# Kernel optimization log

Measured on AMD Instinct MI355X. Metric: run time of the kernel, lower is better.

The kernel has to match this reference:

```python
import jax, jax.numpy as jnp
import numpy as np

N = 20000       # nodes
E = 320000      # edges (without self-loops)
D_IN = 256
HID = 64        # per-head channels, layer 1
HEADS = 4
D_OUT = 256
EPS = 1e-5      # LayerNorm eps
SLOPE = 0.2     # LeakyReLU negative slope (PyG GATConv default)


def setup_inputs() -> dict:
    key = jax.random.key(0)
    ks = jax.random.split(key, 10)
    def glorot(k, shape):
        fan_in, fan_out = shape[0], int(np.prod(shape[1:]))
        s = np.sqrt(2.0 / (fan_in + fan_out)).astype(np.float32)
        return jax.random.normal(k, shape, dtype=jnp.float32) * s
    x = jax.random.normal(ks[0], (N, D_IN), dtype=jnp.float32)
    edge_index = jax.random.randint(ks[1], (2, E), 0, N, dtype=jnp.int64)
    return {
        "x": x,
        "edge_index": edge_index,
        # layer 1: GATConv(D_IN, HID, heads=4, concat=True)
        "W1": glorot(ks[2], (D_IN, HEADS * HID)),
        "a1_src": glorot(ks[3], (HEADS, HID)),
        "a1_dst": glorot(ks[4], (HEADS, HID)),
        "b1": jnp.zeros((HEADS * HID,), jnp.float32),
        # LayerNorm(HEADS*HID)
        "ln_g": jnp.ones((HEADS * HID,), jnp.float32),
        "ln_b": jnp.zeros((HEADS * HID,), jnp.float32),
        # layer 2: GATConv(HEADS*HID, D_OUT, heads=1, concat=False)
        "W2": glorot(ks[5], (HEADS * HID, D_OUT)),
        "a2_src": glorot(ks[6], (1, D_OUT)),
        "a2_dst": glorot(ks[7], (1, D_OUT)),
        "b2": jnp.zeros((D_OUT,), jnp.float32),
    }


def _gat(x, src, dst, W, a_src, a_dst, b, heads, ch, concat):
    """PyG-style GATConv (self-loops already appended to src/dst)."""
    n = x.shape[0]
    h = (x @ W).reshape(n, heads, ch)                      # [n,H,C]
    es = (h * a_src).sum(-1)                               # [n,H] src logits
    ed = (h * a_dst).sum(-1)                               # [n,H] dst logits
    e = jax.nn.leaky_relu(es[src] + ed[dst], SLOPE)        # [Etot,H]
    # softmax over incoming edges of each dst node (stable)
    m = jax.ops.segment_max(e, dst, num_segments=n)
    w = jnp.exp(e - m[dst])
    den = jax.ops.segment_sum(w, dst, num_segments=n)
    alpha = w / den[dst]                                   # [Etot,H]
    msg = h[src] * alpha[:, :, None]                       # [Etot,H,C]
    out = jax.ops.segment_sum(msg, dst, num_segments=n)    # [n,H,C]
    out = out.reshape(n, heads * ch) if concat else out.mean(axis=1)
    return out + b


def _layernorm(x, g, b):
    mu = x.mean(-1, keepdims=True)
    v = ((x - mu) ** 2).mean(-1, keepdims=True)
    return (x - mu) * jax.lax.rsqrt(v + EPS) * g + b


def reference(x, edge_index, W1, a1_src, a1_dst, b1, ln_g, ln_b, W2, a2_src, a2_dst, b2):
    loops = jnp.arange(N, dtype=edge_index.dtype)
    src = jnp.concatenate([edge_index[0], loops])
    dst = jnp.concatenate([edge_index[1], loops])
    h = _gat(x, src, dst, W1, a1_src, a1_dst, b1, HEADS, HID, True)
    h = jax.nn.relu(_layernorm(h, ln_g, ln_b))             # dropout is identity in eval
    out = _gat(h, src, dst, W2, a2_src, a2_dst, b2, 1, D_OUT, False)
    return out
```

## Files before the change

### kernel.cpp

```cpp
#include <hip/hip_runtime.h>
#include <hip/hip_bf16.h>
#include <math.h>

#define N_NODES 20000
#define N_EDGES 320000
#define N_ETOT  (N_EDGES + N_NODES)
#define SLOPE 0.2f
#define LN_EPS 1e-5f
#define APPEND_BLOCKS 1329
#define SLOTS 128

typedef __attribute__((ext_vector_type(8))) short short8v;
typedef __attribute__((ext_vector_type(4))) float f32x4;

__device__ __forceinline__ float lrelu(float x) { return x > 0.f ? x : SLOPE * x; }

__device__ __forceinline__ float rlf(float v, int l) {
  return __uint_as_float(__builtin_amdgcn_readlane(__float_as_uint(v), l));
}
__device__ __forceinline__ int rli(int v, int l) { return __builtin_amdgcn_readlane(v, l); }

__device__ __forceinline__ unsigned short f2bf(float f) {
  __hip_bfloat16 h = __float2bfloat16(f);
  return *reinterpret_cast<unsigned short*>(&h);
}
__device__ __forceinline__ float bf2f(unsigned short u) {
  return __uint_as_float(((unsigned int)u) << 16);
}

__global__ __launch_bounds__(256) void k_init(const float* __restrict__ W1, const float* __restrict__ W2,
                                              unsigned short* __restrict__ P1, unsigned short* __restrict__ P2,
                                              int* __restrict__ deg) {
  int b = blockIdx.x, t = threadIdx.x;
  if (b < 256) {
    int e = b * 256 + t;
    int j = e & 7, lane = (e >> 3) & 63, nf = (e >> 9) & 15, ks = (e >> 13) & 7;
    int col = nf * 16 + (lane & 15);
    int k = ks * 32 + (lane >> 4) * 8 + j;
    P1[e] = f2bf(W1[k * 256 + col]);
    P2[e] = f2bf(W2[k * 256 + col]);
  } else {
    int i = (b - 256) * 256 + t;
    if (i < N_NODES) deg[i] = 0;
  }
}

__global__ __launch_bounds__(256) void k_append_gemm1(const int* __restrict__ ei, int* __restrict__ deg,
                                                      int* __restrict__ srcs,
                                                      const float* __restrict__ x,
                                                      const unsigned short* __restrict__ Wp,
                                                      const float* __restrict__ asrc,
                                                      const float* __restrict__ adst,
                                                      unsigned short* __restrict__ C,
                                                      float* __restrict__ es, float* __restrict__ ed) {
  int b = blockIdx.x, tid = threadIdx.x;
  if (b < APPEND_BLOCKS) {
    int i = b * 256 + tid;
    if (i < N_ETOT) {
      int s, d;
      if (i < N_EDGES) { s = ei[i]; d = ei[N_EDGES + i]; } else { s = i - N_EDGES; d = s; }
      int slot = atomicAdd(&deg[d], 1);
      if (slot < SLOTS) srcs[d * SLOTS + slot] = s;
    }
    return;
  }
  int gwave = (b - APPEND_BLOCKS) * 4 + (tid >> 6);
  if (gwave >= 1250) return;
  int lane = tid & 63;
  int r = lane & 15, kg = lane >> 4;
  int rbase = gwave * 16;

  f32x4 acc[16];
#pragma unroll
  for (int i = 0; i < 16; ++i) acc[i] = (f32x4){0.f, 0.f, 0.f, 0.f};

#pragma unroll
  for (int ks = 0; ks < 8; ++ks) {
    int koff = ks * 32 + kg * 8;
    float4 lo = *reinterpret_cast<const float4*>(&x[(size_t)(rbase + r) * 256 + koff]);
    float4 hi = *reinterpret_cast<const float4*>(&x[(size_t)(rbase + r) * 256 + koff + 4]);
    short8v a;
    a[0] = (short)f2bf(lo.x); a[1] = (short)f2bf(lo.y); a[2] = (short)f2bf(lo.z); a[3] = (short)f2bf(lo.w);
    a[4] = (short)f2bf(hi.x); a[5] = (short)f2bf(hi.y); a[6] = (short)f2bf(hi.z); a[7] = (short)f2bf(hi.w);
#pragma unroll
    for (int nf = 0; nf < 16; ++nf) {
      int4 braw = *reinterpret_cast<const int4*>(&Wp[(size_t)(ks * 16 + nf) * 512 + lane * 8]);
      short8v bfr = __builtin_bit_cast(short8v, braw);
      acc[nf] = __builtin_amdgcn_mfma_f32_16x16x32_bf16(a, bfr, acc[nf], 0, 0, 0);
    }
  }

#pragma unroll
  for (int nf = 0; nf < 16; ++nf) {
#pragma unroll
    for (int q = 0; q < 4; ++q)
      C[(size_t)(rbase + kg * 4 + q) * 256 + nf * 16 + r] = f2bf(acc[nf][q]);
  }

  float as_v[16], ad_v[16];
#pragma unroll
  for (int nf = 0; nf < 16; ++nf) {
    as_v[nf] = asrc[nf * 16 + r];
    ad_v[nf] = adst[nf * 16 + r];
  }
#pragma unroll
  for (int q = 0; q < 4; ++q) {
    float hs[4], hd[4];
#pragma unroll
    for (int h = 0; h < 4; ++h) {
      hs[h] = 0.f; hd[h] = 0.f;
#pragma unroll
      for (int t = 0; t < 4; ++t) {
        int nf = h * 4 + t;
        hs[h] = fmaf(acc[nf][q], as_v[nf], hs[h]);
        hd[h] = fmaf(acc[nf][q], ad_v[nf], hd[h]);
      }
#pragma unroll
      for (int s = 1; s < 16; s <<= 1) {
        hs[h] += __shfl_xor(hs[h], s);
        hd[h] += __shfl_xor(hd[h], s);
      }
    }
    if (r == 0) {
      int row = rbase + kg * 4 + q;
#pragma unroll
      for (int h = 0; h < 4; ++h) {
        es[row * 4 + h] = hs[h];
        ed[row * 4 + h] = hd[h];
      }
    }
  }
}

__global__ __launch_bounds__(256) void k_gat1_gemm2(const unsigned short* __restrict__ h1,
                                                    const float* __restrict__ es, const float* __restrict__ ed,
                                                    const int* __restrict__ degv, const int* __restrict__ srcs,
                                                    const float* __restrict__ b1, const float* __restrict__ lng,
                                                    const float* __restrict__ lnb,
                                                    const unsigned short* __restrict__ Wp,
                                                    const float* __restrict__ a2s, const float* __restrict__ a2d,
                                                    unsigned short* __restrict__ h2b,
                                                    float* __restrict__ es2, float* __restrict__ ed2) {
  __shared__ char hm[16 * 512];
  __shared__ float esp[4][16], edp[4][16];
  int tid = threadIdx.x;
  int w = tid >> 6, lane = tid & 63;
  int myh = lane >> 4;
  int nbase = blockIdx.x * 16;

  for (int i = 0; i < 4; ++i) {
    int lrow = w * 4 + i;
    int n = nbase + lrow;
    int beg = n * SLOTS;
    int deg = degv[n]; deg = deg > SLOTS ? SLOTS : deg;
    float4 edv = *reinterpret_cast<const float4*>(&ed[n * 4]);
    float ax = 0.f, ay = 0.f, az = 0.f, aw = 0.f;
    float invden;

    if (deg <= 64) {
      int sv = 0;
      float e0 = -1e30f, e1 = -1e30f, e2 = -1e30f, e3 = -1e30f;
      bool valid = lane < deg;
      if (valid) {
        sv = srcs[beg + lane];
        float4 esv = *reinterpret_cast<const float4*>(&es[sv * 4]);
        e0 = lrelu(esv.x + edv.x); e1 = lrelu(esv.y + edv.y);
        e2 = lrelu(esv.z + edv.z); e3 = lrelu(esv.w + edv.w);
      }
      float m0 = e0, m1 = e1, m2 = e2, m3 = e3;
#pragma unroll
      for (int s = 1; s < 64; s <<= 1) {
        m0 = fmaxf(m0, __shfl_xor(m0, s)); m1 = fmaxf(m1, __shfl_xor(m1, s));
        m2 = fmaxf(m2, __shfl_xor(m2, s)); m3 = fmaxf(m3, __shfl_xor(m3, s));
      }
      float w0 = valid ? __expf(e0 - m0) : 0.f;
      float w1 = valid ? __expf(e1 - m1) : 0.f;
      float w2 = valid ? __expf(e2 - m2) : 0.f;
      float w3 = valid ? __expf(e3 - m3) : 0.f;
      float d0 = w0, d1 = w1, d2 = w2, d3 = w3;
#pragma unroll
      for (int s = 1; s < 64; s <<= 1) {
        d0 += __shfl_xor(d0, s); d1 += __shfl_xor(d1, s);
        d2 += __shfl_xor(d2, s); d3 += __shfl_xor(d3, s);
      }
      float den = (myh == 0) ? d0 : (myh == 1) ? d1 : (myh == 2) ? d2 : d3;
      invden = 1.f / den;

      int j = 0;
      for (; j + 8 <= deg; j += 8) {
        int ss[8]; ushort4 vv[8];
#pragma unroll
        for (int u = 0; u < 8; ++u) ss[u] = rli(sv, j + u);
#pragma unroll
        for (int u = 0; u < 8; ++u)
          vv[u] = *reinterpret_cast<const ushort4*>(&h1[(size_t)ss[u] * 256 + lane * 4]);
#pragma unroll
        for (int u = 0; u < 8; ++u) {
          int jj = j + u;
          float w0j = rlf(w0, jj), w1j = rlf(w1, jj), w2j = rlf(w2, jj), w3j = rlf(w3, jj);
          float wj = (myh == 0) ? w0j : (myh == 1) ? w1j : (myh == 2) ? w2j : w3j;
          ax = fmaf(wj, bf2f(vv[u].x), ax); ay = fmaf(wj, bf2f(vv[u].y), ay);
          az = fmaf(wj, bf2f(vv[u].z), az); aw = fmaf(wj, bf2f(vv[u].w), aw);
        }
      }
      for (; j + 4 <= deg; j += 4) {
        int ss[4]; ushort4 vv[4];
#pragma unroll
        for (int u = 0; u < 4; ++u) ss[u] = rli(sv, j + u);
#pragma unroll
        for (int u = 0; u < 4; ++u)
          vv[u] = *reinterpret_cast<const ushort4*>(&h1[(size_t)ss[u] * 256 + lane * 4]);
#pragma unroll
        for (int u = 0; u < 4; ++u) {
          int jj = j + u;
          float w0j = rlf(w0, jj), w1j = rlf(w1, jj), w2j = rlf(w2, jj), w3j = rlf(w3, jj);
          float wj = (myh == 0) ? w0j : (myh == 1) ? w1j : (myh == 2) ? w2j : w3j;
          ax = fmaf(wj, bf2f(vv[u].x), ax); ay = fmaf(wj, bf2f(vv[u].y), ay);
          az = fmaf(wj, bf2f(vv[u].z), az); aw = fmaf(wj, bf2f(vv[u].w), aw);
        }
      }
      for (; j < deg; ++j) {
        int sj = rli(sv, j);
        float w0j = rlf(w0, j), w1j = rlf(w1, j), w2j = rlf(w2, j), w3j = rlf(w3, j);
        float wj = (myh == 0) ? w0j : (myh == 1) ? w1j : (myh == 2) ? w2j : w3j;
        ushort4 v = *reinterpret_cast<const ushort4*>(&h1[(size_t)sj * 256 + lane * 4]);
        ax = fmaf(wj, bf2f(v.x), ax); ay = fmaf(wj, bf2f(v.y), ay);
        az = fmaf(wj, bf2f(v.z), az); aw = fmaf(wj, bf2f(v.w), aw);
      }
    } else {
      float m0 = -1e30f, m1 = -1e30f, m2 = -1e30f, m3 = -1e30f;
      for (int j = lane; j < deg; j += 64) {
        int s = srcs[beg + j];
        float4 esv = *reinterpret_cast<const float4*>(&es[s * 4]);
        m0 = fmaxf(m0, lrelu(esv.x + edv.x)); m1 = fmaxf(m1, lrelu(esv.y + edv.y));
        m2 = fmaxf(m2, lrelu(esv.z + edv.z)); m3 = fmaxf(m3, lrelu(esv.w + edv.w));
      }
#pragma unroll
      for (int s = 1; s < 64; s <<= 1) {
        m0 = fmaxf(m0, __shfl_xor(m0, s)); m1 = fmaxf(m1, __shfl_xor(m1, s));
        m2 = fmaxf(m2, __shfl_xor(m2, s)); m3 = fmaxf(m3, __shfl_xor(m3, s));
      }
      float edh = (myh == 0) ? edv.x : (myh == 1) ? edv.y : (myh == 2) ? edv.z : edv.w;
      float mh = (myh == 0) ? m0 : (myh == 1) ? m1 : (myh == 2) ? m2 : m3;
      float den = 0.f;
      for (int j = 0; j < deg; ++j) {
        int s = srcs[beg + j];
        float e = lrelu(es[s * 4 + myh] + edh);
        float wj = __expf(e - mh);
        den += wj;
        ushort4 v = *reinterpret_cast<const ushort4*>(&h1[(size_t)s * 256 + lane * 4]);
        ax = fmaf(wj, bf2f(v.x), ax); ay = fmaf(wj, bf2f(v.y), ay);
        az = fmaf(wj, bf2f(v.z), az); aw = fmaf(wj, bf2f(v.w), aw);
      }
      invden = 1.f / den;
    }

    float4 bb = *reinterpret_cast<const float4*>(&b1[lane * 4]);
    float vx = ax * invden + bb.x, vy = ay * invden + bb.y;
    float vz = az * invden + bb.z, vw = aw * invden + bb.w;
    float sum = vx + vy + vz + vw;
    float sq = vx * vx + vy * vy + vz * vz + vw * vw;
#pragma unroll
    for (int s = 1; s < 64; s <<= 1) { sum += __shfl_xor(sum, s); sq += __shfl_xor(sq, s); }
    float mu = sum * (1.f / 256.f);
    float var = sq * (1.f / 256.f) - mu * mu;
    float rstd = rsqrtf(var + LN_EPS);
    float4 g = *reinterpret_cast<const float4*>(&lng[lane * 4]);
    float4 lb = *reinterpret_cast<const float4*>(&lnb[lane * 4]);
    ushort4 o;
    o.x = f2bf(fmaxf(0.f, (vx - mu) * rstd * g.x + lb.x));
    o.y = f2bf(fmaxf(0.f, (vy - mu) * rstd * g.y + lb.y));
    o.z = f2bf(fmaxf(0.f, (vz - mu) * rstd * g.z + lb.z));
    o.w = f2bf(fmaxf(0.f, (vw - mu) * rstd * g.w + lb.w));
    *reinterpret_cast<ushort4*>(&hm[lrow * 512 + ((lane * 8 + lrow * 64) & 511)]) = o;
  }
  __syncthreads();

  int r = lane & 15, kg = lane >> 4;
  f32x4 acc[4];
#pragma unroll
  for (int i = 0; i < 4; ++i) acc[i] = (f32x4){0.f, 0.f, 0.f, 0.f};

#pragma unroll
  for (int ks = 0; ks < 8; ++ks) {
    int4 araw = *reinterpret_cast<const int4*>(
        &hm[r * 512 + (((ks * 64 + kg * 16) + r * 64) & 511)]);
    short8v a = __builtin_bit_cast(short8v, araw);
#pragma unroll
    for (int nf2 = 0; nf2 < 4; ++nf2) {
      int nf = w * 4 + nf2;
      int4 braw = *reinterpret_cast<const int4*>(&Wp[(size_t)(ks * 16 + nf) * 512 + lane * 8]);
      short8v bfr = __builtin_bit_cast(short8v, braw);
      acc[nf2] = __builtin_amdgcn_mfma_f32_16x16x32_bf16(a, bfr, acc[nf2], 0, 0, 0);
    }
  }

  int rbase = nbase;
#pragma unroll
  for (int nf2 = 0; nf2 < 4; ++nf2) {
#pragma unroll
    for (int q = 0; q < 4; ++q)
      h2b[(size_t)(rbase + kg * 4 + q) * 256 + w * 64 + nf2 * 16 + r] = f2bf(acc[nf2][q]);
  }

  float as_v[4], ad_v[4];
#pragma unroll
  for (int nf2 = 0; nf2 < 4; ++nf2) {
    as_v[nf2] = a2s[w * 64 + nf2 * 16 + r];
    ad_v[nf2] = a2d[w * 64 + nf2 * 16 + r];
  }
#pragma unroll
  for (int q = 0; q < 4; ++q) {
    float s0 = 0.f, d0 = 0.f;
#pragma unroll
    for (int nf2 = 0; nf2 < 4; ++nf2) {
      s0 = fmaf(acc[nf2][q], as_v[nf2], s0);
      d0 = fmaf(acc[nf2][q], ad_v[nf2], d0);
    }
#pragma unroll
    for (int s = 1; s < 16; s <<= 1) {
      s0 += __shfl_xor(s0, s);
      d0 += __shfl_xor(d0, s);
    }
    if (r == 0) {
      esp[w][kg * 4 + q] = s0;
      edp[w][kg * 4 + q] = d0;
    }
  }
  __syncthreads();
  if (tid < 16) {
    es2[rbase + tid] = esp[0][tid] + esp[1][tid] + esp[2][tid] + esp[3][tid];
    ed2[rbase + tid] = edp[0][tid] + edp[1][tid] + edp[2][tid] + edp[3][tid];
  }
}

__global__ __launch_bounds__(256) void k_gat2(const unsigned short* __restrict__ h2,
                                              const float* __restrict__ es, const float* __restrict__ ed,
                                              const int* __restrict__ degv, const int* __restrict__ srcs,
                                              const float* __restrict__ b2, float* __restrict__ out) {
  int n = (blockIdx.x * 256 + threadIdx.x) >> 6;
  if (n >= N_NODES) return;
  int lane = threadIdx.x & 63;
  int beg = n * SLOTS;
  int deg = degv[n]; deg = deg > SLOTS ? SLOTS : deg;
  float edn = ed[n];
  float ax = 0.f, ay = 0.f, az = 0.f, aw = 0.f;
  float invden;

  if (deg <= 64) {
    int sv = 0;
    float e = -1e30f;
    bool valid = lane < deg;
    if (valid) {
      sv = srcs[beg + lane];
      e = lrelu(es[sv] + edn);
    }
    float m = e;
#pragma unroll
    for (int s = 1; s < 64; s <<= 1) m = fmaxf(m, __shfl_xor(m, s));
    float wv = valid ? __expf(e - m) : 0.f;
    float den = wv;
#pragma unroll
    for (int s = 1; s < 64; s <<= 1) den += __shfl_xor(den, s);
    invden = 1.f / den;

    int j = 0;
    for (; j + 8 <= deg; j += 8) {
      int ss[8]; ushort4 vv[8]; float wj[8];
#pragma unroll
      for (int u = 0; u < 8; ++u) ss[u] = rli(sv, j + u);
#pragma unroll
      for (int u = 0; u < 8; ++u)
        vv[u] = *reinterpret_cast<const ushort4*>(&h2[(size_t)ss[u] * 256 + lane * 4]);
#pragma unroll
      for (int u = 0; u < 8; ++u) wj[u] = rlf(wv, j + u);
#pragma unroll
      for (int u = 0; u < 8; ++u) {
        ax = fmaf(wj[u], bf2f(vv[u].x), ax); ay = fmaf(wj[u], bf2f(vv[u].y), ay);
        az = fmaf(wj[u], bf2f(vv[u].z), az); aw = fmaf(wj[u], bf2f(vv[u].w), aw);
      }
    }
    for (; j + 4 <= deg; j += 4) {
      int ss[4]; ushort4 vv[4]; float wj[4];
#pragma unroll
      for (int u = 0; u < 4; ++u) ss[u] = rli(sv, j + u);
#pragma unroll
      for (int u = 0; u < 4; ++u)
        vv[u] = *reinterpret_cast<const ushort4*>(&h2[(size_t)ss[u] * 256 + lane * 4]);
#pragma unroll
      for (int u = 0; u < 4; ++u) wj[u] = rlf(wv, j + u);
#pragma unroll
      for (int u = 0; u < 4; ++u) {
        ax = fmaf(wj[u], bf2f(vv[u].x), ax); ay = fmaf(wj[u], bf2f(vv[u].y), ay);
        az = fmaf(wj[u], bf2f(vv[u].z), az); aw = fmaf(wj[u], bf2f(vv[u].w), aw);
      }
    }
    for (; j < deg; ++j) {
      int sj = rli(sv, j);
      float wj = rlf(wv, j);
      ushort4 v = *reinterpret_cast<const ushort4*>(&h2[(size_t)sj * 256 + lane * 4]);
      ax = fmaf(wj, bf2f(v.x), ax); ay = fmaf(wj, bf2f(v.y), ay);
      az = fmaf(wj, bf2f(v.z), az); aw = fmaf(wj, bf2f(v.w), aw);
    }
  } else {
    float m = -1e30f;
    for (int j = lane; j < deg; j += 64) m = fmaxf(m, lrelu(es[srcs[beg + j]] + edn));
#pragma unroll
    for (int s = 1; s < 64; s <<= 1) m = fmaxf(m, __shfl_xor(m, s));
    float den = 0.f;
    for (int j = 0; j < deg; ++j) {
      int s = srcs[beg + j];
      float wj = __expf(lrelu(es[s] + edn) - m);
      den += wj;
      ushort4 v = *reinterpret_cast<const ushort4*>(&h2[(size_t)s * 256 + lane * 4]);
      ax = fmaf(wj, bf2f(v.x), ax); ay = fmaf(wj, bf2f(v.y), ay);
      az = fmaf(wj, bf2f(v.z), az); aw = fmaf(wj, bf2f(v.w), aw);
    }
    invden = 1.f / den;
  }

  float4 bb = *reinterpret_cast<const float4*>(&b2[lane * 4]);
  float4 o = make_float4(ax * invden + bb.x, ay * invden + bb.y, az * invden + bb.z, aw * invden + bb.w);
  *reinterpret_cast<float4*>(&out[(size_t)n * 256 + lane * 4]) = o;
}

extern "C" void kernel_launch(void* const* d_in, const int* in_sizes, int n_in,
                              void* d_out, int out_size, void* d_ws, size_t ws_size,
                              hipStream_t stream) {
  (void)in_sizes; (void)n_in; (void)out_size; (void)ws_size;
  const float* x   = (const float*)d_in[0];
  const int*   ei  = (const int*)d_in[1];
  const float* W1  = (const float*)d_in[2];
  const float* a1s = (const float*)d_in[3];
  const float* a1d = (const float*)d_in[4];
  const float* b1  = (const float*)d_in[5];
  const float* lng = (const float*)d_in[6];
  const float* lnb = (const float*)d_in[7];
  const float* W2  = (const float*)d_in[8];
  const float* a2s = (const float*)d_in[9];
  const float* a2d = (const float*)d_in[10];
  const float* b2  = (const float*)d_in[11];
  float* out = (float*)d_out;

  char* ws = (char*)d_ws;
  unsigned short* h1b = (unsigned short*)(ws + 0);
  unsigned short* h2b = (unsigned short*)(ws + 10240000);
  unsigned short* Wp1 = (unsigned short*)(ws + 20480000);
  unsigned short* Wp2 = (unsigned short*)(ws + 20611072);
  float* es1 = (float*)(ws + 20742144);
  float* ed1 = (float*)(ws + 21062144);
  float* es2 = (float*)(ws + 21382144);
  float* ed2 = (float*)(ws + 21462144);
  int*   deg = (int*)(ws + 21542144);
  int*   srcs = (int*)(ws + 21622144);

  k_init<<<256 + 79, 256, 0, stream>>>(W1, W2, Wp1, Wp2, deg);
  k_append_gemm1<<<APPEND_BLOCKS + 313, 256, 0, stream>>>(ei, deg, srcs, x, Wp1, a1s, a1d, h1b, es1, ed1);
  k_gat1_gemm2<<<1250, 256, 0, stream>>>(h1b, es1, ed1, deg, srcs, b1, lng, lnb,
                                         Wp2, a2s, a2d, h2b, es2, ed2);
  k_gat2<<<(N_NODES * 64) / 256, 256, 0, stream>>>(h2b, es2, ed2, deg, srcs, b2, out);
}
```

Baseline: 190.7 us.

## Use 1024-thread blocks in fused GAT1+GEMM2 kernel, one wave per node

The fused layer-1 aggregation + LayerNorm + GEMM2 kernel now launches 16 waves per block instead of 4. Each wave aggregates one node rather than looping over four, and in the GEMM phase each wave computes one 16-column MFMA tile instead of four. This exposes more parallelism and memory-level concurrency for the latency-bound gather phase. In exchange it adds a 16-way cross-wave reduction for the attention logits and increases register and LDS pressure per block, which may limit occupancy.

Measured after the change: 201.3 us. 1.06x slower.

```diff
diff --git a/kernel.cpp b/kernel.cpp
--- a/kernel.cpp
+++ b/kernel.cpp
@@ -132,25 +132,24 @@
   }
 }
 
-__global__ __launch_bounds__(256) void k_gat1_gemm2(const unsigned short* __restrict__ h1,
-                                                    const float* __restrict__ es, const float* __restrict__ ed,
-                                                    const int* __restrict__ degv, const int* __restrict__ srcs,
-                                                    const float* __restrict__ b1, const float* __restrict__ lng,
-                                                    const float* __restrict__ lnb,
-                                                    const unsigned short* __restrict__ Wp,
-                                                    const float* __restrict__ a2s, const float* __restrict__ a2d,
-                                                    unsigned short* __restrict__ h2b,
-                                                    float* __restrict__ es2, float* __restrict__ ed2) {
+__global__ __launch_bounds__(1024) void k_gat1_gemm2(const unsigned short* __restrict__ h1,
+                                                     const float* __restrict__ es, const float* __restrict__ ed,
+                                                     const int* __restrict__ degv, const int* __restrict__ srcs,
+                                                     const float* __restrict__ b1, const float* __restrict__ lng,
+                                                     const float* __restrict__ lnb,
+                                                     const unsigned short* __restrict__ Wp,
+                                                     const float* __restrict__ a2s, const float* __restrict__ a2d,
+                                                     unsigned short* __restrict__ h2b,
+                                                     float* __restrict__ es2, float* __restrict__ ed2) {
   __shared__ char hm[16 * 512];
-  __shared__ float esp[4][16], edp[4][16];
+  __shared__ float esp[16][16], edp[16][16];
   int tid = threadIdx.x;
   int w = tid >> 6, lane = tid & 63;
   int myh = lane >> 4;
   int nbase = blockIdx.x * 16;
 
-  for (int i = 0; i < 4; ++i) {
-    int lrow = w * 4 + i;
-    int n = nbase + lrow;
+  {
+    int n = nbase + w;
     int beg = n * SLOTS;
     int deg = degv[n]; deg = deg > SLOTS ? SLOTS : deg;
     float4 edv = *reinterpret_cast<const float4*>(&ed[n * 4]);
@@ -272,51 +271,33 @@
     o.y = f2bf(fmaxf(0.f, (vy - mu) * rstd * g.y + lb.y));
     o.z = f2bf(fmaxf(0.f, (vz - mu) * rstd * g.z + lb.z));
     o.w = f2bf(fmaxf(0.f, (vw - mu) * rstd * g.w + lb.w));
-    *reinterpret_cast<ushort4*>(&hm[lrow * 512 + ((lane * 8 + lrow * 64) & 511)]) = o;
+    *reinterpret_cast<ushort4*>(&hm[w * 512 + ((lane * 8 + w * 64) & 511)]) = o;
   }
   __syncthreads();
 
   int r = lane & 15, kg = lane >> 4;
-  f32x4 acc[4];
-#pragma unroll
-  for (int i = 0; i < 4; ++i) acc[i] = (f32x4){0.f, 0.f, 0.f, 0.f};
+  f32x4 acc = (f32x4){0.f, 0.f, 0.f, 0.f};
 
 #pragma unroll
   for (int ks = 0; ks < 8; ++ks) {
     int4 araw = *reinterpret_cast<const int4*>(
         &hm[r * 512 + (((ks * 64 + kg * 16) + r * 64) & 511)]);
     short8v a = __builtin_bit_cast(short8v, araw);
-#pragma unroll
-    for (int nf2 = 0; nf2 < 4; ++nf2) {
-      int nf = w * 4 + nf2;
-      int4 braw = *reinterpret_cast<const int4*>(&Wp[(size_t)(ks * 16 + nf) * 512 + lane * 8]);
-      short8v bfr = __builtin_bit_cast(short8v, braw);
-      acc[nf2] = __builtin_amdgcn_mfma_f32_16x16x32_bf16(a, bfr, acc[nf2], 0, 0, 0);
-    }
-  }
-
-  int rbase = nbase;
-#pragma unroll
-  for (int nf2 = 0; nf2 < 4; ++nf2) {
-#pragma unroll
-    for (int q = 0; q < 4; ++q)
-      h2b[(size_t)(rbase + kg * 4 + q) * 256 + w * 64 + nf2 * 16 + r] = f2bf(acc[nf2][q]);
-  }
-
-  float as_v[4], ad_v[4];
-#pragma unroll
-  for (int nf2 = 0; nf2 < 4; ++nf2) {
-    as_v[nf2] = a2s[w * 64 + nf2 * 16 + r];
-    ad_v[nf2] = a2d[w * 64 + nf2 * 16 + r];
-  }
+    int4 braw = *reinterpret_cast<const int4*>(&Wp[(size_t)(ks * 16 + w) * 512 + lane * 8]);
+    short8v bfr = __builtin_bit_cast(short8v, braw);
+    acc = __builtin_amdgcn_mfma_f32_16x16x32_bf16(a, bfr, acc, 0, 0, 0);
+  }
+
+#pragma unroll
+  for (int q = 0; q < 4; ++q)
+    h2b[(size_t)(nbase + kg * 4 + q) * 256 + w * 16 + r] = f2bf(acc[q]);
+
+  float as_v = a2s[w * 16 + r];
+  float ad_v = a2d[w * 16 + r];
 #pragma unroll
   for (int q = 0; q < 4; ++q) {
-    float s0 = 0.f, d0 = 0.f;
-#pragma unroll
-    for (int nf2 = 0; nf2 < 4; ++nf2) {
-      s0 = fmaf(acc[nf2][q], as_v[nf2], s0);
-      d0 = fmaf(acc[nf2][q], ad_v[nf2], d0);
-    }
+    float s0 = acc[q] * as_v;
+    float d0 = acc[q] * ad_v;
 #pragma unroll
     for (int s = 1; s < 16; s <<= 1) {
       s0 += __shfl_xor(s0, s);
@@ -329,8 +310,11 @@
   }
   __syncthreads();
   if (tid < 16) {
-    es2[rbase + tid] = esp[0][tid] + esp[1][tid] + esp[2][tid] + esp[3][tid];
-    ed2[rbase + tid] = edp[0][tid] + edp[1][tid] + edp[2][tid] + edp[3][tid];
+    float se = 0.f, de = 0.f;
+#pragma unroll
+    for (int u = 0; u < 16; ++u) { se += esp[u][tid]; de += edp[u][tid]; }
+    es2[nbase + tid] = se;
+    ed2[nbase + tid] = de;
   }
 }
 
@@ -456,7 +440,7 @@
 
   k_init<<<256 + 79, 256, 0, stream>>>(W1, W2, Wp1, Wp2, deg);
   k_append_gemm1<<<APPEND_BLOCKS + 313, 256, 0, stream>>>(ei, deg, srcs, x, Wp1, a1s, a1d, h1b, es1, ed1);
-  k_gat1_gemm2<<<1250, 256, 0, stream>>>(h1b, es1, ed1, deg, srcs, b1, lng, lnb,
-                                         Wp2, a2s, a2d, h2b, es2, ed2);
+  k_gat1_gemm2<<<1250, 1024, 0, stream>>>(h1b, es1, ed1, deg, srcs, b1, lng, lnb,
+                                          Wp2, a2s, a2d, h2b, es2, ed2);
   k_gat2<<<(N_NODES * 64) / 256, 256, 0, stream>>>(h2b, es2, ed2, deg, srcs, b2, out);
 }
```
